# Optimization experiments

Hardware: AMD Instinct MI355X
Metric: run time of the kernel (lower is better)

## Reference

```python
import jax, jax.numpy as jnp
import numpy as np

N, K, D = 16384, 200, 64  # n_samples, n_components, n_features (8x8 patches)
LOG_2PI = np.float32(np.log(2.0 * np.pi))


def setup_inputs() -> dict:
    rng = np.random.default_rng(0)
    # Build SPD covariances and derive precisions_cholesky exactly like the module:
    # cov_chol = cholesky(cov, lower); prec_chol = solve(cov_chol, I).T
    A = rng.normal(size=(K, D, D))
    cov = A @ A.transpose(0, 2, 1) + D * np.eye(D)  # well-conditioned SPD
    cov_chol = np.linalg.cholesky(cov)  # lower triangular [K,D,D]
    eye = np.broadcast_to(np.eye(D), (K, D, D))
    prec_chol = np.linalg.solve(cov_chol, eye).transpose(0, 2, 1).astype(np.float32)
    means = rng.normal(size=(K, D)).astype(np.float32)
    key = jax.random.key(0)
    x = jax.random.normal(key, (N, D), dtype=jnp.float32)
    return {"x": x, "means": jnp.asarray(means), "prec_chol": jnp.asarray(prec_chol)}


def reference(x, means, prec_chol):
    """Batched GMM log-prob (fused version of estimate_log_prob_torch).

    log_prob[n,k] = -0.5*(D*log(2pi) + ||x_n L_k - mu_k L_k||^2) + log|det L_k|
    where L_k = precisions_cholesky[k].
    """
    n_features = x.shape[1]
    # y[n,k,e] = x @ L_k  -- one batched GEMM instead of K small matmuls
    y = jnp.einsum('nd,kde->nke', x, prec_chol)
    mu_prec = jnp.einsum('kd,kde->ke', means, prec_chol)  # mu_k @ L_k, [K,D]
    log_prob = jnp.sum(jnp.square(y - mu_prec[None, :, :]), axis=-1)  # [N,K]
    # log det of cholesky of precision = sum of log of diagonal entries
    log_det = jnp.sum(jnp.log(jnp.diagonal(prec_chol, axis1=1, axis2=2)), axis=1)  # [K]
    return -0.5 * (n_features * LOG_2PI + log_prob) + log_det[None, :]
```

## Files before the change

kernel.cpp:

```cpp
#include <hip/hip_runtime.h>
#include <hip/hip_bf16.h>
#include <stdint.h>

typedef __bf16 bf16x8 __attribute__((ext_vector_type(8)));
typedef float  f32x4  __attribute__((ext_vector_type(4)));
typedef float  f32x2  __attribute__((ext_vector_type(2)));
typedef float  f32x16 __attribute__((ext_vector_type(16)));

#define KC 200
#define KB 8
#define CBASE (-58.8120661251f)


__global__ __launch_bounds__(256) void prep_b(const float* __restrict__ prec,
                                              const float* __restrict__ means,
                                              __bf16* __restrict__ Lt,
                                              float* __restrict__ muL,
                                              float* __restrict__ ckh) {
    __shared__ float sP[64][40];
    __shared__ float sM[64];
    const int k = blockIdx.x >> 1, h = blockIdx.x & 1, tid = threadIdx.x;
    const float* pk = prec + (size_t)k * 4096 + h * 32;
    #pragma unroll
    for (int it = 0; it < 2; ++it) {
        int f4 = tid + it * 256;
        int d = f4 >> 3, c = (f4 & 7) * 4;
        float4 v = *(const float4*)(pk + (size_t)d * 64 + c);
        *(float4*)&sP[d][c] = v;
    }
    if (tid < 16) *(float4*)&sM[tid * 4] = ((const float4*)(means + (size_t)k * 64))[tid];
    __syncthreads();
    {
        int e = tid >> 3, d0 = (tid & 7) * 8;
        bf16x8 o;
        #pragma unroll
        for (int i = 0; i < 8; ++i) o[i] = (__bf16)sP[d0 + i][e];
        *(bf16x8*)(Lt + (size_t)k * 4096 + (size_t)(h * 32 + e) * 64 + d0) = o;
    }
    if (tid < 32) {
        int e = tid;
        float m = 0.f;
        #pragma unroll 8
        for (int d = 0; d < 64; ++d) m = fmaf(sM[d], sP[d][e], m);
        muL[k * 64 + h * 32 + e] = m;
        float l = __logf(sP[h * 32 + e][e]);
        #pragma unroll
        for (int mm = 16; mm >= 1; mm >>= 1) l += __shfl_xor(l, mm, 64);
        if (e == 0) ckh[h * KC + k] = l;
    }
}

#define GLL16(gp_, lp_) \
    __builtin_amdgcn_global_load_lds((__attribute__((address_space(1))) const void*)(gp_), \
                                     (__attribute__((address_space(3))) void*)(lp_), 16, 0, 0)

__global__ __launch_bounds__(256, 4) void gmm_main(const float* __restrict__ x,
                                                   const __bf16* __restrict__ Lt,
                                                   const float* __restrict__ muL,
                                                   const float* __restrict__ ckh,
                                                   float* __restrict__ out) {
    __shared__ __align__(16) __bf16 sB[2 * 4096];
    __shared__ __align__(16) float  sOutT[KB][256];
    __shared__ float sCk[KB];

    const int tid  = threadIdx.x;
    const int wave = tid >> 6, lane = tid & 63;
    const int hp   = lane >> 5;
    const int l31  = lane & 31;
    const int r8   = lane >> 3, s8 = lane & 7;
    const int row0 = blockIdx.x * 256;
    const int rowW = row0 + wave * 64;
    const int k0   = blockIdx.y * KB;
    char* sBc = (char*)sB;

    {
        const __bf16* L0 = Lt + (size_t)k0 * 4096;
        #pragma unroll
        for (int i = 0; i < 2; ++i) {
            int t = wave * 2 + i;
            GLL16(L0 + (size_t)(t * 8 + r8) * 64 + (s8 ^ r8) * 8, sBc + t * 1024);
        }
    }
    if (tid < KB) sCk[tid] = ckh[k0 + tid] + ckh[KC + k0 + tid] + CBASE;

    bf16x8 mubv[2];
    #pragma unroll
    for (int et = 0; et < 2; ++et)
        #pragma unroll
        for (int kk = 0; kk < KB; ++kk) {
            float v = muL[(size_t)(k0 + kk) * 64 + et * 32 + l31];
            mubv[et][kk] = (hp == 0) ? (__bf16)v : (__bf16)0.f;
        }
    bf16x8 afmu = (bf16x8)(__bf16)0.f;
    afmu[0] = (hp == 0) ? (__bf16)(-1.0f) : (__bf16)0.f;

    bf16x8 af[2][4];
    #pragma unroll
    for (int rt = 0; rt < 2; ++rt) {
        const float* xr = x + (size_t)(rowW + 32 * rt + l31) * 64 + 8 * hp;
        #pragma unroll
        for (int ki = 0; ki < 4; ++ki) {
            float4 v0 = *(const float4*)(xr + 16 * ki);
            float4 v1 = *(const float4*)(xr + 16 * ki + 4);
            bf16x8 a;
            a[0] = (__bf16)v0.x; a[1] = (__bf16)v0.y; a[2] = (__bf16)v0.z; a[3] = (__bf16)v0.w;
            a[4] = (__bf16)v1.x; a[5] = (__bf16)v1.y; a[6] = (__bf16)v1.z; a[7] = (__bf16)v1.w;
            af[rt][ki] = a;
        }
    }

    #pragma unroll
    for (int kk = 0; kk < KB; ++kk) {
        __syncthreads();
        if (kk + 1 < KB) {
            const __bf16* Ln = Lt + (size_t)(k0 + kk + 1) * 4096;
            char* dst = sBc + ((kk & 1) ^ 1) * 8192;
            #pragma unroll
            for (int i = 0; i < 2; ++i) {
                int t = wave * 2 + i;
                GLL16(Ln + (size_t)(t * 8 + r8) * 64 + (s8 ^ r8) * 8, dst + t * 1024);
            }
        }
        const char* buf = sBc + (kk & 1) * 8192;
        f32x2 p2[2] = {(f32x2){0.f, 0.f}, (f32x2){0.f, 0.f}};

        #pragma unroll
        for (int et = 0; et < 2; ++et) {
            const int e = et * 32 + l31;
            bf16x8 lf[4];
            #pragma unroll
            for (int ki = 0; ki < 4; ++ki) {
                int slot = (2 * ki + hp) ^ (lane & 7);
                lf[ki] = *(const bf16x8*)(buf + e * 128 + (slot << 4));
            }
            bf16x8 lfmu = (bf16x8)(__bf16)0.f;
            lfmu[0] = mubv[et][kk];

            f32x16 acc[2];
            #pragma unroll
            for (int rt = 0; rt < 2; ++rt) {
                acc[rt] = __builtin_amdgcn_mfma_f32_32x32x16_bf16(
                    lfmu, afmu, (f32x16)0.f, 0, 0, 0);
                #pragma unroll
                for (int ki = 0; ki < 4; ++ki)
                    acc[rt] = __builtin_amdgcn_mfma_f32_32x32x16_bf16(
                        lf[ki], af[rt][ki], acc[rt], 0, 0, 0);
            }
            #pragma unroll
            for (int rt = 0; rt < 2; ++rt)
                #pragma unroll
                for (int i = 0; i < 8; ++i) {
                    f32x2 pa = {acc[rt][2 * i], acc[rt][2 * i + 1]};
                    p2[rt] += pa * pa;
                }
        }
        float pr0 = p2[0][0] + p2[0][1];
        float pr1 = p2[1][0] + p2[1][1];
        pr0 += __shfl_xor(pr0, 32, 64);
        pr1 += __shfl_xor(pr1, 32, 64);
        float val = hp ? pr1 : pr0;
        sOutT[kk][wave * 64 + lane] = fmaf(-0.5f, val, sCk[kk]);
    }
    __syncthreads();

    {
        float vals[KB];
        #pragma unroll
        for (int kk = 0; kk < KB; ++kk) vals[kk] = sOutT[kk][tid];
        f32x4 a = {vals[0], vals[1], vals[2], vals[3]};
        f32x4 b = {vals[4], vals[5], vals[6], vals[7]};
        float* op = out + (size_t)(row0 + tid) * KC + k0;
        *(f32x4*)op = a;
        *(f32x4*)(op + 4) = b;
    }
}

extern "C" void kernel_launch(void* const* d_in, const int* in_sizes, int n_in,
                              void* d_out, int out_size, void* d_ws, size_t ws_size,
                              hipStream_t stream) {
    const float* x     = (const float*)d_in[0];
    const float* means = (const float*)d_in[1];
    const float* prec  = (const float*)d_in[2];
    float* out = (float*)d_out;

    __bf16* Lt  = (__bf16*)d_ws;
    float*  muL = (float*)((char*)d_ws + 1638400);
    float*  ckh = (float*)((char*)d_ws + 1689600);

    prep_b<<<400, 256, 0, stream>>>(prec, means, Lt, muL, ckh);
    gmm_main<<<dim3(64, KC / KB), 256, 0, stream>>>(x, Lt, muL, ckh, out);
}
```

Before: 105.6 us.

## Stage bf16 x tile in LDS and keep per-wave precision factors in registers

The prep kernel now also converts x to bf16 in a workspace buffer and writes the precision matrices in an MFMA-fragment-ready layout. The main kernel loads the whole 256-row bf16 x tile into LDS once, and each wave owns two components whose L fragments are loaded straight from global into registers. The mean offset is folded into the MFMA accumulator initialisation, replacing the extra mu MFMA. This removes the per-component double-buffered LDS pipeline and the fp32 x conversion in the main kernel, at the cost of a larger LDS footprint (32KB for x) and an extra x round trip through global memory.

```diff
diff --git a/kernel.cpp b/kernel.cpp
--- a/kernel.cpp
+++ b/kernel.cpp
@@ -2,24 +2,39 @@
 #include <hip/hip_bf16.h>
 #include <stdint.h>
 
-typedef __bf16 bf16x8 __attribute__((ext_vector_type(8)));
-typedef float  f32x4  __attribute__((ext_vector_type(4)));
-typedef float  f32x2  __attribute__((ext_vector_type(2)));
-typedef float  f32x16 __attribute__((ext_vector_type(16)));
+typedef __bf16 bf16x4v __attribute__((ext_vector_type(4)));
+typedef __bf16 bf16x8  __attribute__((ext_vector_type(8)));
+typedef float  f32x4   __attribute__((ext_vector_type(4)));
+typedef float  f32x2   __attribute__((ext_vector_type(2)));
+typedef float  f32x16  __attribute__((ext_vector_type(16)));
 
 #define KC 200
 #define KB 8
 #define CBASE (-58.8120661251f)
 
 
-__global__ __launch_bounds__(256) void prep_b(const float* __restrict__ prec,
-                                              const float* __restrict__ means,
-                                              __bf16* __restrict__ Lt,
-                                              float* __restrict__ muL,
-                                              float* __restrict__ ckh) {
+__global__ __launch_bounds__(256) void prep(const float* __restrict__ prec,
+                                            const float* __restrict__ means,
+                                            const float* __restrict__ x,
+                                            __bf16* __restrict__ Ltf,
+                                            float* __restrict__ muL,
+                                            float* __restrict__ ckh,
+                                            __bf16* __restrict__ xb) {
+    const int tid = threadIdx.x;
+    if (blockIdx.x >= 400) {
+        const size_t base = (size_t)(blockIdx.x - 400) * 4096;
+        #pragma unroll
+        for (int r = 0; r < 4; ++r) {
+            size_t idx = base + r * 1024 + tid * 4;
+            float4 v = *(const float4*)(x + idx);
+            bf16x4v o = {(__bf16)v.x, (__bf16)v.y, (__bf16)v.z, (__bf16)v.w};
+            *(bf16x4v*)(xb + idx) = o;
+        }
+        return;
+    }
     __shared__ float sP[64][40];
     __shared__ float sM[64];
-    const int k = blockIdx.x >> 1, h = blockIdx.x & 1, tid = threadIdx.x;
+    const int k = blockIdx.x >> 1, h = blockIdx.x & 1;
     const float* pk = prec + (size_t)k * 4096 + h * 32;
     #pragma unroll
     for (int it = 0; it < 2; ++it) {
@@ -31,11 +46,12 @@
     if (tid < 16) *(float4*)&sM[tid * 4] = ((const float4*)(means + (size_t)k * 64))[tid];
     __syncthreads();
     {
-        int e = tid >> 3, d0 = (tid & 7) * 8;
+        int lane = tid & 63, ki = tid >> 6;
+        int hp = lane >> 5, l31 = lane & 31;
         bf16x8 o;
         #pragma unroll
-        for (int i = 0; i < 8; ++i) o[i] = (__bf16)sP[d0 + i][e];
-        *(bf16x8*)(Lt + (size_t)k * 4096 + (size_t)(h * 32 + e) * 64 + d0) = o;
+        for (int j = 0; j < 8; ++j) o[j] = (__bf16)sP[16 * ki + 8 * hp + j][l31];
+        *(bf16x8*)(Ltf + (size_t)k * 4096 + (h * 4 + ki) * 512 + lane * 8) = o;
     }
     if (tid < 32) {
         int e = tid;
@@ -54,14 +70,13 @@
     __builtin_amdgcn_global_load_lds((__attribute__((address_space(1))) const void*)(gp_), \
                                      (__attribute__((address_space(3))) void*)(lp_), 16, 0, 0)
 
-__global__ __launch_bounds__(256, 4) void gmm_main(const float* __restrict__ x,
-                                                   const __bf16* __restrict__ Lt,
+__global__ __launch_bounds__(256, 4) void gmm_main(const __bf16* __restrict__ xb,
+                                                   const __bf16* __restrict__ Ltf,
                                                    const float* __restrict__ muL,
                                                    const float* __restrict__ ckh,
                                                    float* __restrict__ out) {
-    __shared__ __align__(16) __bf16 sB[2 * 4096];
+    __shared__ __align__(16) __bf16 sX[256 * 64];
     __shared__ __align__(16) float  sOutT[KB][256];
-    __shared__ float sCk[KB];
 
     const int tid  = threadIdx.x;
     const int wave = tid >> 6, lane = tid & 63;
@@ -69,97 +84,63 @@
     const int l31  = lane & 31;
     const int r8   = lane >> 3, s8 = lane & 7;
     const int row0 = blockIdx.x * 256;
-    const int rowW = row0 + wave * 64;
     const int k0   = blockIdx.y * KB;
-    char* sBc = (char*)sB;
-
-    {
-        const __bf16* L0 = Lt + (size_t)k0 * 4096;
-        #pragma unroll
-        for (int i = 0; i < 2; ++i) {
-            int t = wave * 2 + i;
-            GLL16(L0 + (size_t)(t * 8 + r8) * 64 + (s8 ^ r8) * 8, sBc + t * 1024);
-        }
-    }
-    if (tid < KB) sCk[tid] = ckh[k0 + tid] + ckh[KC + k0 + tid] + CBASE;
-
-    bf16x8 mubv[2];
-    #pragma unroll
-    for (int et = 0; et < 2; ++et)
-        #pragma unroll
-        for (int kk = 0; kk < KB; ++kk) {
-            float v = muL[(size_t)(k0 + kk) * 64 + et * 32 + l31];
-            mubv[et][kk] = (hp == 0) ? (__bf16)v : (__bf16)0.f;
-        }
-    bf16x8 afmu = (bf16x8)(__bf16)0.f;
-    afmu[0] = (hp == 0) ? (__bf16)(-1.0f) : (__bf16)0.f;
-
-    bf16x8 af[2][4];
-    #pragma unroll
-    for (int rt = 0; rt < 2; ++rt) {
-        const float* xr = x + (size_t)(rowW + 32 * rt + l31) * 64 + 8 * hp;
-        #pragma unroll
-        for (int ki = 0; ki < 4; ++ki) {
-            float4 v0 = *(const float4*)(xr + 16 * ki);
-            float4 v1 = *(const float4*)(xr + 16 * ki + 4);
-            bf16x8 a;
-            a[0] = (__bf16)v0.x; a[1] = (__bf16)v0.y; a[2] = (__bf16)v0.z; a[3] = (__bf16)v0.w;
-            a[4] = (__bf16)v1.x; a[5] = (__bf16)v1.y; a[6] = (__bf16)v1.z; a[7] = (__bf16)v1.w;
-            af[rt][ki] = a;
-        }
-    }
+    char* sXc = (char*)sX;
 
     #pragma unroll
-    for (int kk = 0; kk < KB; ++kk) {
-        __syncthreads();
-        if (kk + 1 < KB) {
-            const __bf16* Ln = Lt + (size_t)(k0 + kk + 1) * 4096;
-            char* dst = sBc + ((kk & 1) ^ 1) * 8192;
+    for (int i = 0; i < 8; ++i) {
+        int t = wave * 8 + i;
+        GLL16(xb + (size_t)(row0 + t * 8 + r8) * 64 + (s8 ^ r8) * 8, sXc + t * 1024);
+    }
+    __syncthreads();
+
+    #pragma unroll
+    for (int ks = 0; ks < 2; ++ks) {
+        const int k  = k0 + wave * 2 + ks;
+        const int kl = wave * 2 + ks;
+        bf16x8 lf[2][4];
+        #pragma unroll
+        for (int et = 0; et < 2; ++et)
             #pragma unroll
-            for (int i = 0; i < 2; ++i) {
-                int t = wave * 2 + i;
-                GLL16(Ln + (size_t)(t * 8 + r8) * 64 + (s8 ^ r8) * 8, dst + t * 1024);
+            for (int ki = 0; ki < 4; ++ki)
+                lf[et][ki] = *(const bf16x8*)(Ltf + (size_t)k * 4096 + (et * 4 + ki) * 512 + lane * 8);
+        f32x16 c0[2];
+        #pragma unroll
+        for (int et = 0; et < 2; ++et)
+            #pragma unroll
+            for (int q2 = 0; q2 < 4; ++q2) {
+                f32x4 m = *(const f32x4*)(muL + (size_t)k * 64 + et * 32 + 8 * q2 + 4 * hp);
+                c0[et][4 * q2 + 0] = -m[0]; c0[et][4 * q2 + 1] = -m[1];
+                c0[et][4 * q2 + 2] = -m[2]; c0[et][4 * q2 + 3] = -m[3];
             }
-        }
-        const char* buf = sBc + (kk & 1) * 8192;
-        f32x2 p2[2] = {(f32x2){0.f, 0.f}, (f32x2){0.f, 0.f}};
+        const float ck = ckh[k] + ckh[KC + k] + CBASE;
 
         #pragma unroll
-        for (int et = 0; et < 2; ++et) {
-            const int e = et * 32 + l31;
-            bf16x8 lf[4];
+        for (int rt = 0; rt < 8; ++rt) {
+            bf16x8 xf[4];
             #pragma unroll
-            for (int ki = 0; ki < 4; ++ki) {
-                int slot = (2 * ki + hp) ^ (lane & 7);
-                lf[ki] = *(const bf16x8*)(buf + e * 128 + (slot << 4));
+            for (int ki = 0; ki < 4; ++ki)
+                xf[ki] = *(const bf16x8*)(sXc + (rt * 32 + l31) * 128
+                                          + (((2 * ki + hp) ^ (l31 & 7)) << 4));
+            f32x16 a0 = __builtin_amdgcn_mfma_f32_32x32x16_bf16(lf[0][0], xf[0], c0[0], 0, 0, 0);
+            f32x16 a1 = __builtin_amdgcn_mfma_f32_32x32x16_bf16(lf[1][0], xf[0], c0[1], 0, 0, 0);
+            #pragma unroll
+            for (int ki = 1; ki < 4; ++ki) {
+                a0 = __builtin_amdgcn_mfma_f32_32x32x16_bf16(lf[0][ki], xf[ki], a0, 0, 0, 0);
+                a1 = __builtin_amdgcn_mfma_f32_32x32x16_bf16(lf[1][ki], xf[ki], a1, 0, 0, 0);
             }
-            bf16x8 lfmu = (bf16x8)(__bf16)0.f;
-            lfmu[0] = mubv[et][kk];
-
-            f32x16 acc[2];
+            f32x2 p2 = {0.f, 0.f};
             #pragma unroll
-            for (int rt = 0; rt < 2; ++rt) {
-                acc[rt] = __builtin_amdgcn_mfma_f32_32x32x16_bf16(
-                    lfmu, afmu, (f32x16)0.f, 0, 0, 0);
-                #pragma unroll
-                for (int ki = 0; ki < 4; ++ki)
-                    acc[rt] = __builtin_amdgcn_mfma_f32_32x32x16_bf16(
-                        lf[ki], af[rt][ki], acc[rt], 0, 0, 0);
+            for (int i = 0; i < 8; ++i) {
+                f32x2 u = {a0[2 * i], a0[2 * i + 1]};
+                f32x2 v = {a1[2 * i], a1[2 * i + 1]};
+                p2 += u * u;
+                p2 += v * v;
             }
-            #pragma unroll
-            for (int rt = 0; rt < 2; ++rt)
-                #pragma unroll
-                for (int i = 0; i < 8; ++i) {
-                    f32x2 pa = {acc[rt][2 * i], acc[rt][2 * i + 1]};
-                    p2[rt] += pa * pa;
-                }
+            float pr = p2[0] + p2[1];
+            pr += __shfl_xor(pr, 32, 64);
+            if (hp == 0) sOutT[kl][rt * 32 + l31] = fmaf(-0.5f, pr, ck);
         }
-        float pr0 = p2[0][0] + p2[0][1];
-        float pr1 = p2[1][0] + p2[1][1];
-        pr0 += __shfl_xor(pr0, 32, 64);
-        pr1 += __shfl_xor(pr1, 32, 64);
-        float val = hp ? pr1 : pr0;
-        sOutT[kk][wave * 64 + lane] = fmaf(-0.5f, val, sCk[kk]);
     }
     __syncthreads();
 
@@ -183,10 +164,11 @@
     const float* prec  = (const float*)d_in[2];
     float* out = (float*)d_out;
 
-    __bf16* Lt  = (__bf16*)d_ws;
+    __bf16* Ltf = (__bf16*)d_ws;
     float*  muL = (float*)((char*)d_ws + 1638400);
     float*  ckh = (float*)((char*)d_ws + 1689600);
+    __bf16* xb  = (__bf16*)((char*)d_ws + 1691200);
 
-    prep_b<<<400, 256, 0, stream>>>(prec, means, Lt, muL, ckh);
-    gmm_main<<<dim3(64, KC / KB), 256, 0, stream>>>(x, Lt, muL, ckh, out);
+    prep<<<656, 256, 0, stream>>>(prec, means, x, Ltf, muL, ckh, xb);
+    gmm_main<<<dim3(64, KC / KB), 256, 0, stream>>>(xb, Ltf, muL, ckh, out);
 }
```

Measured after the change: 93.90 us. 1.12x faster.
